# Performance work log

Hardware: AMD Instinct MI355X
Metric: run time of the kernel (lower is better)

## Reference

```python
import jax, jax.numpy as jnp
import numpy as np
from functools import partial

B, E, H, M, NUM_NODES = 256, 256, 256, 128, 512


def _uni(key, shape, fan):
    bound = 1.0 / np.sqrt(fan)
    return jax.random.uniform(key, shape, jnp.float32, -bound, bound)


def setup_inputs() -> dict:
    key = jax.random.key(0)
    ks = jax.random.split(key, 12)
    return {
        "emb": jax.random.normal(ks[0], (B, E), jnp.float32),
        # FNN: Linear(E->H) + relu + Linear(H->H)  (num_layers=2, no batch norm)
        "fnn_w1": _uni(ks[1], (H, E), E),
        "fnn_b1": _uni(ks[2], (H,), E),
        "fnn_w2": _uni(ks[3], (H, H), H),
        "fnn_b2": _uni(ks[4], (H,), H),
        # GRUCell(input_size=H, hidden_size=H), torch layout: [3H, H] in (r,z,n) order
        "gru_w_ih": _uni(ks[5], (3 * H, H), H),
        "gru_b_ih": _uni(ks[6], (3 * H,), H),
        "gru_w_hh": _uni(ks[7], (3 * H, H), H),
        "gru_b_hh": _uni(ks[8], (3 * H,), H),
        # out_linear: Linear(H -> M)
        "out_w": _uni(ks[9], (M, H), H),
        "out_b": _uni(ks[10], (M,), H),
    }


def _gru_cell(x, h, w_ih, b_ih, w_hh, b_hh):
    # torch.nn.GRUCell math, gates in (r, z, n) order
    gi = x @ w_ih.T + b_ih            # [B, 3H]
    gh = h @ w_hh.T + b_hh            # [B, 3H]
    i_r, i_z, i_n = jnp.split(gi, 3, axis=-1)
    h_r, h_z, h_n = jnp.split(gh, 3, axis=-1)
    r = jax.nn.sigmoid(i_r + h_r)
    z = jax.nn.sigmoid(i_z + h_z)
    n = jnp.tanh(i_n + r * h_n)
    return (1.0 - z) * n + z * h


def reference(emb, fnn_w1, fnn_b1, fnn_w2, fnn_b2,
              gru_w_ih, gru_b_ih, gru_w_hh, gru_b_hh, out_w, out_b):
    # FNN: relu between layers, linear output
    hx = jax.nn.relu(emb @ fnn_w1.T + fnn_b1)
    hx = hx @ fnn_w2.T + fnn_b2                      # [B, H]

    cell = partial(_gru_cell, w_ih=gru_w_ih, b_ih=gru_b_ih,
                   w_hh=gru_w_hh, b_hh=gru_b_hh)

    def step(carry, _):
        h, prev_out = carry                           # input to cell is previous output
        h_new = cell(prev_out, h)
        return (h_new, h_new), h_new

    init = (hx, jnp.zeros_like(hx))                   # first input is zeros_like(hx)
    (hx_final, _), ys = jax.lax.scan(step, init, None, length=NUM_NODES)
    x = jnp.transpose(ys, (1, 0, 2))                  # [B, NUM_NODES, H]
    x = x @ out_w.T + out_b                           # [B, NUM_NODES, M]
    return (x, hx_final)
```

## Files before the change

### kernel.cpp

```cpp
#include <hip/hip_runtime.h>
#include <stdint.h>

#define BATCH 256
#define HDIM  256
#define MDIM  128
#define NSTEPS 512

typedef unsigned short u16;
typedef unsigned int   u32;
typedef short short8 __attribute__((ext_vector_type(8)));
typedef float f32x4  __attribute__((ext_vector_type(4)));
typedef u32 u32x4 __attribute__((ext_vector_type(4)));

__device__ __forceinline__ u16 f2bf(float f) {
    u32 x = __builtin_bit_cast(u32, f);
    u32 r = x + 0x7FFFu + ((x >> 16) & 1u);
    return (u16)(r >> 16);
}
__device__ __forceinline__ float bf2f(u16 h) {
    u32 x = ((u32)h) << 16;
    return __builtin_bit_cast(float, x);
}
__device__ __forceinline__ float sigm(float x) { return 1.f / (1.f + __expf(-x)); }
__device__ __forceinline__ float tanh_f(float x) {
    float ax = fabsf(x);
    float e  = __expf(-2.f * ax);
    float t  = (1.f - e) / (1.f + e);
    return copysignf(t, x);
}
__device__ __forceinline__ f32x4 mfma16(short8 a, short8 b, f32x4 c) {
    return __builtin_amdgcn_mfma_f32_16x16x32_bf16(a, b, c, 0, 0, 0);
}

#define CLOAD_L2(dst, p, OFS)                                                  \
    asm volatile("global_load_dwordx4 %0, %1, off offset:" OFS " sc0"          \
                 : "=v"(dst) : "v"(p) : "memory")
#define CLOAD_SYS(dst, p, OFS)                                                 \
    asm volatile("global_load_dwordx4 %0, %1, off offset:" OFS " sc0 sc1"      \
                 : "=v"(dst) : "v"(p) : "memory")
#define CSTORE_LOC(p, v)                                                       \
    asm volatile("global_store_dword %0, %1, off"                              \
                 :: "v"(p), "v"(v) : "memory")
#define CSTORE_SYS(p, v)                                                       \
    asm volatile("global_store_dword %0, %1, off sc0 sc1"                      \
                 :: "v"(p), "v"(v) : "memory")

#define ISSUE16(MACRO, v, base)                                                \
    MACRO(v[0],  base, "0");   MACRO(v[1],  base, "16");                       \
    MACRO(v[2],  base, "128"); MACRO(v[3],  base, "144");                      \
    MACRO(v[4],  base, "256"); MACRO(v[5],  base, "272");                      \
    MACRO(v[6],  base, "384"); MACRO(v[7],  base, "400");                      \
    MACRO(v[8],  base, "512"); MACRO(v[9],  base, "528");                      \
    MACRO(v[10], base, "640"); MACRO(v[11], base, "656");                      \
    MACRO(v[12], base, "768"); MACRO(v[13], base, "784");                      \
    MACRO(v[14], base, "896"); MACRO(v[15], base, "912")

__device__ __forceinline__ void spin_load(const u32* baseL, const u32* baseM,
                                          u32 tag, short8 a[8]) {
    for (int it = 0;; ++it) {
        u32x4 v[16];
        const bool sys = (it & 1);
        if (sys) { ISSUE16(CLOAD_SYS, v, baseM); }
        else     { ISSUE16(CLOAD_L2,  v, baseL); }
        asm volatile("s_waitcnt vmcnt(0)" ::: "memory");
        __builtin_amdgcn_sched_barrier(0);
        bool ok = true;
#pragma unroll
        for (int i = 0; i < 16; ++i)
#pragma unroll
            for (int j = 0; j < 4; ++j) ok = ok && ((v[i][j] >> 16) == tag);
        if (__all((int)ok)) {
#pragma unroll
            for (int kt = 0; kt < 8; ++kt)
#pragma unroll
                for (int j = 0; j < 8; ++j)
                    a[kt][j] = (short)(v[2 * kt + (j >> 2)][j & 3] & 0xFFFFu);
            return;
        }
        if (sys) __builtin_amdgcn_s_sleep(1);
    }
}

__global__ __launch_bounds__(256) void k_prep(
    const float* __restrict__ w_ih, const float* __restrict__ w_hh,
    const float* __restrict__ b_ih, const float* __restrict__ b_hh,
    const float* __restrict__ ow,   const float* __restrict__ obv,
    u16* __restrict__ Whi, u16* __restrict__ Wlo, float* __restrict__ bias,
    u32* __restrict__ exch) {
    int row = blockIdx.x;
    int c   = threadIdx.x;
    float v;
    if (row < 512)        v = w_ih[row * HDIM + c] + w_hh[row * HDIM + c];
    else if (row < 768)   v = w_ih[row * HDIM + c];
    else if (row < 1024)  v = w_hh[(row - 256) * HDIM + c];
    else                  v = ow[(row - 1024) * HDIM + c];
    u16 hi = f2bf(v);
    u16 lo = f2bf(v - bf2f(hi));
    Whi[(size_t)row * HDIM + c] = hi;
    Wlo[(size_t)row * HDIM + c] = lo;
    if (c == 0) {
        float bv;
        if (row < 512)        bv = b_ih[row] + b_hh[row];
        else if (row < 768)   bv = b_ih[row];
        else if (row < 1024)  bv = b_hh[row - 256];
        else                  bv = obv[row - 1024];
        bias[row] = bv;
    }
    if (row < 1024) exch[row * 256 + c] = 0u;
}

template <int RELU>
__global__ __launch_bounds__(256) void k_gemm_f32(
    const float* __restrict__ A, const float* __restrict__ W,
    const float* __restrict__ bvec, float* __restrict__ out, int N, int K) {
    __shared__ float At[16][17];
    __shared__ float Wt[16][17];
    int tx = threadIdx.x, ty = threadIdx.y;
    int mrow = blockIdx.x * 16 + ty;
    int nrow = blockIdx.y * 16 + ty;
    float acc = 0.0f;
    for (int k0 = 0; k0 < K; k0 += 16) {
        At[ty][tx] = A[(size_t)mrow * K + k0 + tx];
        Wt[ty][tx] = W[(size_t)nrow * K + k0 + tx];
        __syncthreads();
#pragma unroll
        for (int kk = 0; kk < 16; ++kk) acc += At[ty][kk] * Wt[tx][kk];
        __syncthreads();
    }
    int n = blockIdx.y * 16 + tx;
    float r = acc + bvec[n];
    if (RELU) r = fmaxf(r, 0.0f);
    out[(size_t)mrow * N + n] = r;
}

__global__ __launch_bounds__(64, 1) void k_scan(
    const u16* __restrict__ Whi, const u16* __restrict__ Wlo,
    const float* __restrict__ bias,
    const float* __restrict__ hx, const float* __restrict__ w_hh,
    const float* __restrict__ b_ih, const float* __restrict__ b_hh,
    u32* __restrict__ exch, float* __restrict__ out1, float* __restrict__ out2) {

    const int b    = blockIdx.x;
    const int w    = b >> 4;
    const int g    = ((b & 7) << 1) | ((b >> 3) & 1);
    const int lane = threadIdx.x;
    const int col_l = lane & 15;
    const int kgrp  = lane >> 4;
    const int kofs  = kgrp * 8;
    const int r0    = kgrp * 4;
    const int jcol  = w * 16 + col_l;
    const int pcol  = (w & 7) * 16 + col_l;
    const int myt   = w >> 3;

    short8 bhi[4][8], blo[4][8], phi[8];
#pragma unroll
    for (int g4 = 0; g4 < 4; ++g4) {
        const u16* base_hi = Whi + (size_t)(g4 * 256 + jcol) * HDIM;
        const u16* base_lo = Wlo + (size_t)(g4 * 256 + jcol) * HDIM;
#pragma unroll
        for (int kt = 0; kt < 8; ++kt) {
            bhi[g4][kt] = *(const short8*)(base_hi + kt * 32 + kofs);
            blo[g4][kt] = *(const short8*)(base_lo + kt * 32 + kofs);
        }
    }
    {
        const u16* base_p = Whi + (size_t)(1024 + pcol) * HDIM;
#pragma unroll
        for (int kt = 0; kt < 8; ++kt)
            phi[kt] = *(const short8*)(base_p + kt * 32 + kofs);
    }

    const float b_r  = bias[jcol];
    const float b_z  = bias[256 + jcol];
    const float b_in = bias[512 + jcol];
    const float b_hn = bias[768 + jcol];
    const float ob   = bias[1024 + pcol];

    u32* const L0 = exch + (size_t)(0 * 16 + g) * 4096;
    u32* const L1 = exch + (size_t)(1 * 16 + g) * 4096;
    u32* const M0 = exch + 131072 + (size_t)(0 * 16 + g) * 4096;
    u32* const M1 = exch + 131072 + (size_t)(1 * 16 + g) * 4096;
    const int rd_off = col_l * 256 + kofs;
    const int wr_off = r0 * 256 + jcol;

    float hold[4];
    {
        float ghr[4] = {0, 0, 0, 0}, ghz[4] = {0, 0, 0, 0}, ghn[4] = {0, 0, 0, 0};
        const float* wr_ = w_hh + (size_t)jcol * HDIM;
        const float* wz_ = w_hh + (size_t)(256 + jcol) * HDIM;
        const float* wn_ = w_hh + (size_t)(512 + jcol) * HDIM;
        const float* hx0 = hx + (size_t)(g * 16 + r0) * HDIM;
        for (int k = 0; k < HDIM; ++k) {
            float fr = wr_[k], fz = wz_[k], fn = wn_[k];
#pragma unroll
            for (int i = 0; i < 4; ++i) {
                float h = hx0[i * HDIM + k];
                ghr[i] += h * fr; ghz[i] += h * fz; ghn[i] += h * fn;
            }
        }
#pragma unroll
        for (int i = 0; i < 4; ++i) {
            float rr = sigm(b_ih[jcol] + b_hh[jcol] + ghr[i]);
            float zz = sigm(b_ih[256 + jcol] + b_hh[256 + jcol] + ghz[i]);
            float nn = tanh_f(b_ih[512 + jcol] + rr * (ghn[i] + b_hh[512 + jcol]));
            float hv = nn + zz * (hx0[i * HDIM + jcol] - nn);
            hold[i] = hv;
            u32 pk = (1u << 16) | (u32)f2bf(hv);
            CSTORE_LOC(L1 + wr_off + i * 256, pk);
            CSTORE_SYS(M1 + wr_off + i * 256, pk);
        }
    }

    f32x4 opend;
    int   tpend = -1;
    for (int s = 1; s <= 511; ++s) {
        const u32* einL = ((s & 1) ? L1 : L0) + rd_off;
        const u32* einM = ((s & 1) ? M1 : M0) + rd_off;
        u32*      eoutL = ((s & 1) ? L0 : L1) + wr_off;
        u32*      eoutM = ((s & 1) ? M0 : M1) + wr_off;

        short8 a[8];
        spin_load(einL, einM, (u32)s, a);

        if (tpend >= 0) {
#pragma unroll
            for (int i = 0; i < 4; ++i)
                __builtin_nontemporal_store(
                    opend[i] + ob,
                    out1 + (size_t)(g * 16 + r0 + i) * (NSTEPS * MDIM) +
                        (size_t)tpend * MDIM + pcol);
        }

        f32x4 acc[4];
#pragma unroll
        for (int n = 0; n < 4; ++n) acc[n] = (f32x4){0.f, 0.f, 0.f, 0.f};
#pragma unroll
        for (int kt = 0; kt < 8; ++kt)
#pragma unroll
            for (int g4 = 0; g4 < 4; ++g4) {
                acc[g4] = mfma16(a[kt], bhi[g4][kt], acc[g4]);
                acc[g4] = mfma16(a[kt], blo[g4][kt], acc[g4]);
            }

        u32 pk[4];
#pragma unroll
        for (int i = 0; i < 4; ++i) {
            float rr = sigm(acc[0][i] + b_r);
            float zz = sigm(acc[1][i] + b_z);
            float nn = tanh_f(acc[2][i] + b_in + rr * (acc[3][i] + b_hn));
            float hv = nn + zz * (hold[i] - nn);
            hold[i] = hv;
            pk[i] = ((u32)(s + 1) << 16) | (u32)f2bf(hv);
        }
#pragma unroll
        for (int i = 0; i < 4; ++i) CSTORE_LOC(eoutL + i * 256, pk[i]);
#pragma unroll
        for (int i = 0; i < 4; ++i) CSTORE_SYS(eoutM + i * 256, pk[i]);

        const int t = s - 1;
        if ((t & 1) == myt) {
            f32x4 oacc = (f32x4){0.f, 0.f, 0.f, 0.f};
#pragma unroll
            for (int kt = 0; kt < 8; ++kt) oacc = mfma16(a[kt], phi[kt], oacc);
            opend = oacc;
            tpend = t;
        }
    }

    if (tpend >= 0) {
#pragma unroll
        for (int i = 0; i < 4; ++i)
            __builtin_nontemporal_store(
                opend[i] + ob,
                out1 + (size_t)(g * 16 + r0 + i) * (NSTEPS * MDIM) +
                    (size_t)tpend * MDIM + pcol);
    }

    if (myt == 1) {
        short8 a[8];
        spin_load(L0 + rd_off, M0 + rd_off, 512u, a);
        f32x4 oacc = (f32x4){0.f, 0.f, 0.f, 0.f};
#pragma unroll
        for (int kt = 0; kt < 8; ++kt) oacc = mfma16(a[kt], phi[kt], oacc);
#pragma unroll
        for (int i = 0; i < 4; ++i)
            __builtin_nontemporal_store(
                oacc[i] + ob,
                out1 + (size_t)(g * 16 + r0 + i) * (NSTEPS * MDIM) +
                    511ull * MDIM + pcol);
    }

#pragma unroll
    for (int i = 0; i < 4; ++i)
        __builtin_nontemporal_store(
            hold[i], out2 + (size_t)(g * 16 + r0 + i) * HDIM + jcol);
}

extern "C" void kernel_launch(void* const* d_in, const int* in_sizes, int n_in,
                              void* d_out, int out_size, void* d_ws, size_t ws_size,
                              hipStream_t stream) {
    const float* P[11];
    for (int i = 0; i < 11 && i < n_in; ++i) P[i] = (const float*)d_in[i];

    const float *emb, *w1, *b1, *w2, *b2, *w_ih, *b_ih, *w_hh, *b_hh, *ow, *obv;
    if (n_in > 1 && in_sizes[1] == 256) {
        emb = P[0]; b1 = P[1]; b2 = P[2]; w1 = P[3]; w2 = P[4];
        b_hh = P[5]; b_ih = P[6]; w_hh = P[7]; w_ih = P[8];
        obv = P[9]; ow = P[10];
    } else if (n_in > 1 && in_sizes[1] == 32768) {
        obv = P[0]; ow = P[1]; b_hh = P[2]; w_hh = P[3]; b_ih = P[4];
        w_ih = P[5]; b2 = P[6]; w2 = P[7]; b1 = P[8]; w1 = P[9]; emb = P[10];
    } else {
        emb = P[0]; w1 = P[1]; b1 = P[2]; w2 = P[3]; b2 = P[4];
        w_ih = P[5]; b_ih = P[6]; w_hh = P[7]; b_hh = P[8];
        ow = P[9]; obv = P[10];
    }

    float* out1 = (float*)d_out;
    float* out2 = out1 + (size_t)BATCH * NSTEPS * MDIM;

    char* ws = (char*)d_ws;
    u16*   Whi  = (u16*)(ws + 0);
    u16*   Wlo  = (u16*)(ws + 589824);
    float* bias = (float*)(ws + 1179648);
    u32*   exch = (u32*)(ws + 1184256);
    float* mid  = (float*)(ws + 2232832);
    float* hxb  = (float*)(ws + 2494976);

    k_prep<<<1152, 256, 0, stream>>>(w_ih, w_hh, b_ih, b_hh, ow, obv,
                                     Whi, Wlo, bias, exch);
    k_gemm_f32<1><<<dim3(16, 16), dim3(16, 16), 0, stream>>>(emb, w1, b1, mid, 256, 256);
    k_gemm_f32<0><<<dim3(16, 16), dim3(16, 16), 0, stream>>>(mid, w2, b2, hxb, 256, 256);
    k_scan<<<256, 64, 0, stream>>>(Whi, Wlo, bias, hxb, w_hh, b_ih, b_hh,
                                   exch, out1, out2);
}
```

Measured before the change: 1.728 ms.

## Assign scan work by runtime XCD id and poll L2 more often

The scan kernel no longer derives its batch-group and column-slice ids from blockIdx. Each block reads its XCD id from a hardware register and atomically claims a slot on that XCD. Blocks that find their XCD full wait until all 256 have arrived and then take any free id with compare-exchange. The intent is to keep blocks that exchange data through the spin-wait on the same XCD, so most polls hit the shared L2 instead of crossing dies. The spin loop now uses the system-coherent load only every fourth iteration instead of every other. This adds a startup handshake and claim buffer, and the wait for all 256 blocks assumes every block is co-resident.

New measurement: 2.436 ms. 1.41x slower.

```diff
diff --git a/kernel.cpp b/kernel.cpp
--- a/kernel.cpp
+++ b/kernel.cpp
@@ -59,7 +59,7 @@
                                           u32 tag, short8 a[8]) {
     for (int it = 0;; ++it) {
         u32x4 v[16];
-        const bool sys = (it & 1);
+        const bool sys = ((it & 3) == 3);
         if (sys) { ISSUE16(CLOAD_SYS, v, baseM); }
         else     { ISSUE16(CLOAD_L2,  v, baseL); }
         asm volatile("s_waitcnt vmcnt(0)" ::: "memory");
@@ -86,7 +86,7 @@
     const float* __restrict__ b_ih, const float* __restrict__ b_hh,
     const float* __restrict__ ow,   const float* __restrict__ obv,
     u16* __restrict__ Whi, u16* __restrict__ Wlo, float* __restrict__ bias,
-    u32* __restrict__ exch) {
+    u32* __restrict__ exch, u32* __restrict__ claim) {
     int row = blockIdx.x;
     int c   = threadIdx.x;
     float v;
@@ -107,6 +107,8 @@
         bias[row] = bv;
     }
     if (row < 1024) exch[row * 256 + c] = 0u;
+    if (row == 1024) claim[c] = 0u;
+    if (row == 1025 && c < 16) claim[256 + c] = 0u;
 }
 
 template <int RELU>
@@ -138,12 +140,51 @@
     const float* __restrict__ bias,
     const float* __restrict__ hx, const float* __restrict__ w_hh,
     const float* __restrict__ b_ih, const float* __restrict__ b_hh,
-    u32* __restrict__ exch, float* __restrict__ out1, float* __restrict__ out2) {
-
-    const int b    = blockIdx.x;
-    const int w    = b >> 4;
-    const int g    = ((b & 7) << 1) | ((b >> 3) & 1);
+    u32* __restrict__ exch, u32* __restrict__ claim,
+    float* __restrict__ out1, float* __restrict__ out2) {
+
     const int lane = threadIdx.x;
+
+    u32 myid;
+    {
+        u32 xcd;
+        asm volatile("s_getreg_b32 %0, hwreg(HW_REG_XCC_ID)" : "=s"(xcd));
+        xcd &= 7u;
+        u32 id = 0xFFFFFFFFu;
+        if (lane == 0) {
+            u32 slot = __hip_atomic_fetch_add(&claim[256 + xcd], 1u,
+                                              __ATOMIC_RELAXED,
+                                              __HIP_MEMORY_SCOPE_AGENT);
+            if (slot < 32u) {
+                id = xcd * 32u + slot;
+                __hip_atomic_store(&claim[id], 1u, __ATOMIC_RELAXED,
+                                   __HIP_MEMORY_SCOPE_AGENT);
+            }
+            __hip_atomic_fetch_add(&claim[264], 1u, __ATOMIC_RELEASE,
+                                   __HIP_MEMORY_SCOPE_AGENT);
+            if (id == 0xFFFFFFFFu) {
+                while (__hip_atomic_load(&claim[264], __ATOMIC_ACQUIRE,
+                                         __HIP_MEMORY_SCOPE_AGENT) < 256u)
+                    __builtin_amdgcn_s_sleep(2);
+                for (u32 cand = 0;; cand = (cand + 1u) & 255u) {
+                    if (__hip_atomic_load(&claim[cand], __ATOMIC_RELAXED,
+                                          __HIP_MEMORY_SCOPE_AGENT) == 0u) {
+                        u32 exp = 0u;
+                        if (__hip_atomic_compare_exchange_strong(
+                                &claim[cand], &exp, 1u, __ATOMIC_RELAXED,
+                                __ATOMIC_RELAXED, __HIP_MEMORY_SCOPE_AGENT)) {
+                            id = cand;
+                            break;
+                        }
+                    }
+                }
+            }
+        }
+        myid = (u32)__shfl((int)id, 0);
+    }
+    const int g = (myid >> 5) * 2 + ((myid >> 4) & 1);
+    const int w = myid & 15;
+
     const int col_l = lane & 15;
     const int kgrp  = lane >> 4;
     const int kofs  = kgrp * 8;
@@ -320,17 +361,18 @@
     float* out2 = out1 + (size_t)BATCH * NSTEPS * MDIM;
 
     char* ws = (char*)d_ws;
-    u16*   Whi  = (u16*)(ws + 0);
-    u16*   Wlo  = (u16*)(ws + 589824);
-    float* bias = (float*)(ws + 1179648);
-    u32*   exch = (u32*)(ws + 1184256);
-    float* mid  = (float*)(ws + 2232832);
-    float* hxb  = (float*)(ws + 2494976);
+    u16*   Whi   = (u16*)(ws + 0);
+    u16*   Wlo   = (u16*)(ws + 589824);
+    float* bias  = (float*)(ws + 1179648);
+    u32*   exch  = (u32*)(ws + 1184256);
+    u32*   claim = (u32*)(ws + 2232832);
+    float* mid   = (float*)(ws + 2236928);
+    float* hxb   = (float*)(ws + 2499072);
 
     k_prep<<<1152, 256, 0, stream>>>(w_ih, w_hh, b_ih, b_hh, ow, obv,
-                                     Whi, Wlo, bias, exch);
+                                     Whi, Wlo, bias, exch, claim);
     k_gemm_f32<1><<<dim3(16, 16), dim3(16, 16), 0, stream>>>(emb, w1, b1, mid, 256, 256);
     k_gemm_f32<0><<<dim3(16, 16), dim3(16, 16), 0, stream>>>(mid, w2, b2, hxb, 256, 256);
     k_scan<<<256, 64, 0, stream>>>(Whi, Wlo, bias, hxb, w_hh, b_ih, b_hh,
-                                   exch, out1, out2);
-}
+                                   exch, claim, out1, out2);
+}
```
